# Kernel optimization log

Measured on AMD Instinct MI355X. Metric: run time of the kernel, lower is better.

The kernel has to match this reference:

```python
import jax, jax.numpy as jnp
import numpy as np

ALPHA = 0.4  # EMARecurrent(alpha=0.4, learnable=False); forward uses |alpha|


def setup_inputs() -> dict:
    key = jax.random.key(0)
    k1, _ = jax.random.split(key)
    inp = jax.random.normal(k1, (8, 1024, 4096), dtype=jnp.float32)  # [B, D, T]
    hidden = jnp.zeros((8, 1024, 1), dtype=jnp.float32)              # [B, D, 1]
    return {"inp": inp, "hidden": hidden}


def reference(inp, hidden):
    # hidden_t = |a| * x_t + (1 - |a|) * hidden_{t-1}, scanned over axis 2.
    a = jnp.abs(jnp.asarray(ALPHA, dtype=inp.dtype))
    xs = jnp.moveaxis(inp, 2, 0)          # [T, B, D]
    h0 = jnp.squeeze(hidden, axis=2)      # [B, D]

    def step(h, x):
        h = a * x + (1.0 - a) * h
        return h, h

    _, ys = jax.lax.scan(step, h0, xs)    # ys: [T, B, D]
    return jnp.moveaxis(ys, 0, 2)         # [B, D, T]
```

## Files before the change

### kernel.cpp

```cpp
#include <hip/hip_runtime.h>


constexpr int STILES_PER_SEQ = 8;

__global__ __launch_bounds__(256) void ema_tile_kernel(
    const float* __restrict__ x,
    const float* __restrict__ h0,
    float* __restrict__ out,
    int ntiles)
{
    const int gtid = blockIdx.x * blockDim.x + threadIdx.x;
    const int w    = gtid >> 6;
    const int lane = threadIdx.x & 63;
    if (w >= ntiles) return;

    const int sidx = w & (STILES_PER_SEQ - 1);
    const int seq  = w >> 3;

    const float a   = 0.4f;
    const float b   = 0.6f;
    const float b2  = b * b;
    const float b3  = b2 * b;
    const float b4  = b2 * b2;
    const float b8  = b4 * b4;
    const float b16 = b8 * b8;
    const float inv_b4 = 1.0f / b4;

    const float m1 = (lane >= 1) ? b4  : 0.0f;
    const float m2 = (lane >= 2) ? b8  : 0.0f;
    const float m3 = (lane >= 4) ? b16 : 0.0f;
    const float pb4i = exp2f((float)(4 * lane) * -0.73696559416f);

    const float4* __restrict__ xp = (const float4*)x;
    float4* __restrict__ op       = (float4*)out;

    const size_t base = (size_t)w * 128;

    float4 vA = xp[base + (size_t)lane];
    float4 vB = xp[base + 64 + (size_t)lane];

    const bool has_warm = (sidx != 0);
    float4 wv = make_float4(0.f, 0.f, 0.f, 0.f);
    if (has_warm && lane < 8) {
        wv = xp[base - 8 + (size_t)lane];
    }

    float a0 = a * vA.x;
    float a1 = fmaf(b, a0, a * vA.y);
    float a2 = fmaf(b, a1, a * vA.z);
    float a3 = fmaf(b, a2, a * vA.w);

    float c0 = a * vB.x;
    float c1 = fmaf(b, c0, a * vB.y);
    float c2 = fmaf(b, c1, a * vB.z);
    float c3 = fmaf(b, c2, a * vB.w);

    float d0 = a * wv.x;
    float d1 = fmaf(b, d0, a * wv.y);
    float d2 = fmaf(b, d1, a * wv.z);
    float d3 = fmaf(b, d2, a * wv.w);

    float tA = a3, tB = c3, tw = d3, u;
    u = __shfl_up(tA, 1, 64); tA = fmaf(m1, u, tA);
    u = __shfl_up(tB, 1, 64); tB = fmaf(m1, u, tB);
    u = __shfl_up(tw, 1, 64); tw = fmaf(m1, u, tw);
    u = __shfl_up(tA, 2, 64); tA = fmaf(m2, u, tA);
    u = __shfl_up(tB, 2, 64); tB = fmaf(m2, u, tB);
    u = __shfl_up(tw, 2, 64); tw = fmaf(m2, u, tw);
    u = __shfl_up(tA, 4, 64); tA = fmaf(m3, u, tA);
    u = __shfl_up(tB, 4, 64); tB = fmaf(m3, u, tB);
    u = __shfl_up(tw, 4, 64); tw = fmaf(m3, u, tw);

    float h_in;
    if (has_warm) {
        h_in = __shfl(tw, 7, 64);
    } else {
        h_in = h0[(size_t)seq];
    }

    float eA = fmaf(pb4i, h_in, (tA - a3) * inv_b4);
    float4 oA;
    oA.x = fmaf(b , eA, a0);
    oA.y = fmaf(b2, eA, a1);
    oA.z = fmaf(b3, eA, a2);
    oA.w = fmaf(b4, eA, a3);

    float h_mid = __shfl(oA.w, 63, 64);

    float eB = fmaf(pb4i, h_mid, (tB - c3) * inv_b4);
    float4 oB;
    oB.x = fmaf(b , eB, c0);
    oB.y = fmaf(b2, eB, c1);
    oB.z = fmaf(b3, eB, c2);
    oB.w = fmaf(b4, eB, c3);

    op[base + (size_t)lane]      = oA;
    op[base + 64 + (size_t)lane] = oB;
}

extern "C" void kernel_launch(void* const* d_in, const int* in_sizes, int n_in,
                              void* d_out, int out_size, void* d_ws, size_t ws_size,
                              hipStream_t stream) {
    const float* x  = (const float*)d_in[0];
    const float* h0 = (const float*)d_in[1];
    float* out = (float*)d_out;

    const int nseq   = in_sizes[1];
    const int ntiles = nseq * STILES_PER_SEQ;
    const int block  = 256;
    const long long total = (long long)ntiles * 64;
    const int grid = (int)((total + block - 1) / block);

    ema_tile_kernel<<<grid, block, 0, stream>>>(x, h0, out, ntiles);
}
```

Measured before the change: 228.6 us.

## Process whole sequence per wavefront with carried state instead of warm-up tiles

Each wavefront now scans a full 4096-step sequence in eight chunks of 512 steps. It carries the running hidden state between chunks through a cross-lane broadcast, replacing independent tiles that each rebuilt their starting state from a 32-element warm-up window. The next chunk is prefetched one iteration ahead. This removes the redundant warm-up loads and shuffles and makes the result exact rather than truncated. The cost is a grid eight times smaller and a serial dependency across chunks, which may reduce memory-level parallelism.

Result: no change. 232.2 us (+1.6%).

```diff
diff --git a/kernel.cpp b/kernel.cpp
--- a/kernel.cpp
+++ b/kernel.cpp
@@ -1,21 +1,18 @@
 #include <hip/hip_runtime.h>
 
 
-constexpr int STILES_PER_SEQ = 8;
+constexpr int T4 = 1024;
 
-__global__ __launch_bounds__(256) void ema_tile_kernel(
+__global__ __launch_bounds__(256) void ema_seq_kernel(
     const float* __restrict__ x,
     const float* __restrict__ h0,
     float* __restrict__ out,
-    int ntiles)
+    int nseq)
 {
     const int gtid = blockIdx.x * blockDim.x + threadIdx.x;
     const int w    = gtid >> 6;
     const int lane = threadIdx.x & 63;
-    if (w >= ntiles) return;
-
-    const int sidx = w & (STILES_PER_SEQ - 1);
-    const int seq  = w >> 3;
+    if (w >= nseq) return;
 
     const float a   = 0.4f;
     const float b   = 0.6f;
@@ -31,71 +28,61 @@
     const float m3 = (lane >= 4) ? b16 : 0.0f;
     const float pb4i = exp2f((float)(4 * lane) * -0.73696559416f);
 
-    const float4* __restrict__ xp = (const float4*)x;
-    float4* __restrict__ op       = (float4*)out;
+    const float4* __restrict__ xp = (const float4*)x   + (size_t)w * T4 + (size_t)lane;
+    float4* __restrict__ op       = (float4*)out       + (size_t)w * T4 + (size_t)lane;
 
-    const size_t base = (size_t)w * 128;
+    float h = h0[(size_t)w];
 
-    float4 vA = xp[base + (size_t)lane];
-    float4 vB = xp[base + 64 + (size_t)lane];
+    float4 vA = xp[0];
+    float4 vB = xp[64];
 
-    const bool has_warm = (sidx != 0);
-    float4 wv = make_float4(0.f, 0.f, 0.f, 0.f);
-    if (has_warm && lane < 8) {
-        wv = xp[base - 8 + (size_t)lane];
+    #pragma unroll
+    for (int it = 0; it < 8; ++it) {
+        float4 nA = vA, nB = vB;
+        if (it < 7) { nA = xp[128]; nB = xp[192]; }
+
+        float a0 = a * vA.x;
+        float a1 = fmaf(b, a0, a * vA.y);
+        float a2 = fmaf(b, a1, a * vA.z);
+        float a3 = fmaf(b, a2, a * vA.w);
+
+        float c0 = a * vB.x;
+        float c1 = fmaf(b, c0, a * vB.y);
+        float c2 = fmaf(b, c1, a * vB.z);
+        float c3 = fmaf(b, c2, a * vB.w);
+
+        float tA = a3, tB = c3, u;
+        u = __shfl_up(tA, 1, 64); tA = fmaf(m1, u, tA);
+        u = __shfl_up(tB, 1, 64); tB = fmaf(m1, u, tB);
+        u = __shfl_up(tA, 2, 64); tA = fmaf(m2, u, tA);
+        u = __shfl_up(tB, 2, 64); tB = fmaf(m2, u, tB);
+        u = __shfl_up(tA, 4, 64); tA = fmaf(m3, u, tA);
+        u = __shfl_up(tB, 4, 64); tB = fmaf(m3, u, tB);
+
+        float eA = fmaf(pb4i, h, (tA - a3) * inv_b4);
+        float4 oA;
+        oA.x = fmaf(b , eA, a0);
+        oA.y = fmaf(b2, eA, a1);
+        oA.z = fmaf(b3, eA, a2);
+        oA.w = fmaf(b4, eA, a3);
+
+        float h_mid = __shfl(oA.w, 63, 64);
+
+        float eB = fmaf(pb4i, h_mid, (tB - c3) * inv_b4);
+        float4 oB;
+        oB.x = fmaf(b , eB, c0);
+        oB.y = fmaf(b2, eB, c1);
+        oB.z = fmaf(b3, eB, c2);
+        oB.w = fmaf(b4, eB, c3);
+
+        op[0]  = oA;
+        op[64] = oB;
+
+        h = __shfl(oB.w, 63, 64);
+
+        vA = nA; vB = nB;
+        xp += 128; op += 128;
     }
-
-    float a0 = a * vA.x;
-    float a1 = fmaf(b, a0, a * vA.y);
-    float a2 = fmaf(b, a1, a * vA.z);
-    float a3 = fmaf(b, a2, a * vA.w);
-
-    float c0 = a * vB.x;
-    float c1 = fmaf(b, c0, a * vB.y);
-    float c2 = fmaf(b, c1, a * vB.z);
-    float c3 = fmaf(b, c2, a * vB.w);
-
-    float d0 = a * wv.x;
-    float d1 = fmaf(b, d0, a * wv.y);
-    float d2 = fmaf(b, d1, a * wv.z);
-    float d3 = fmaf(b, d2, a * wv.w);
-
-    float tA = a3, tB = c3, tw = d3, u;
-    u = __shfl_up(tA, 1, 64); tA = fmaf(m1, u, tA);
-    u = __shfl_up(tB, 1, 64); tB = fmaf(m1, u, tB);
-    u = __shfl_up(tw, 1, 64); tw = fmaf(m1, u, tw);
-    u = __shfl_up(tA, 2, 64); tA = fmaf(m2, u, tA);
-    u = __shfl_up(tB, 2, 64); tB = fmaf(m2, u, tB);
-    u = __shfl_up(tw, 2, 64); tw = fmaf(m2, u, tw);
-    u = __shfl_up(tA, 4, 64); tA = fmaf(m3, u, tA);
-    u = __shfl_up(tB, 4, 64); tB = fmaf(m3, u, tB);
-    u = __shfl_up(tw, 4, 64); tw = fmaf(m3, u, tw);
-
-    float h_in;
-    if (has_warm) {
-        h_in = __shfl(tw, 7, 64);
-    } else {
-        h_in = h0[(size_t)seq];
-    }
-
-    float eA = fmaf(pb4i, h_in, (tA - a3) * inv_b4);
-    float4 oA;
-    oA.x = fmaf(b , eA, a0);
-    oA.y = fmaf(b2, eA, a1);
-    oA.z = fmaf(b3, eA, a2);
-    oA.w = fmaf(b4, eA, a3);
-
-    float h_mid = __shfl(oA.w, 63, 64);
-
-    float eB = fmaf(pb4i, h_mid, (tB - c3) * inv_b4);
-    float4 oB;
-    oB.x = fmaf(b , eB, c0);
-    oB.y = fmaf(b2, eB, c1);
-    oB.z = fmaf(b3, eB, c2);
-    oB.w = fmaf(b4, eB, c3);
-
-    op[base + (size_t)lane]      = oA;
-    op[base + 64 + (size_t)lane] = oB;
 }
 
 extern "C" void kernel_launch(void* const* d_in, const int* in_sizes, int n_in,
@@ -105,11 +92,10 @@
     const float* h0 = (const float*)d_in[1];
     float* out = (float*)d_out;
 
-    const int nseq   = in_sizes[1];
-    const int ntiles = nseq * STILES_PER_SEQ;
-    const int block  = 256;
-    const long long total = (long long)ntiles * 64;
+    const int nseq  = in_sizes[1];
+    const int block = 256;
+    const long long total = (long long)nseq * 64;
     const int grid = (int)((total + block - 1) / block);
 
-    ema_tile_kernel<<<grid, block, 0, stream>>>(x, h0, out, ntiles);
+    ema_seq_kernel<<<grid, block, 0, stream>>>(x, h0, out, nseq);
 }
```
